# Kernel tuning notes

Measured on AMD Instinct MI355X. Metric: run time of the kernel, lower is better.

Reference implementation:

```python
import jax, jax.numpy as jnp
import numpy as np

# Dimensions (see shape_source)
L = 1024   # episode_len (memory slots)
B = 64     # batch (parallel envs)
K = 512    # key_size
V = 512    # value_size
H = 8      # num_head
MEMB = 256 # memory_state_embedding
SDIM = 512 # state_dim
HID = 512  # hidden width of all 2-layer encoders
RIMQ = 512 # rim_query_size
LAT = K - MEMB  # task_inference_latent dim


def setup_inputs() -> dict:
    key = jax.random.key(0)
    ks = jax.random.split(key, 16)
    w = lambda k, shape: (jax.random.normal(k, shape, jnp.float32) * 0.02)
    return {
        "state": jax.random.normal(ks[0], (B, SDIM), jnp.float32),
        "task_inference_latent": jax.random.normal(ks[1], (B, LAT), jnp.float32),
        "keys": jax.random.normal(ks[2], (L, B, K), jnp.float32),
        "vals": jax.random.normal(ks[3], (L, B, V), jnp.float32),
        "rpe_mod": jax.random.uniform(ks[4], (L, B, 1), jnp.float32),
        "step": jnp.maximum(jax.random.randint(ks[5], (B,), 0, L), 1),
        "W_state": w(ks[6], (SDIM, MEMB)), "b_state": jnp.zeros((MEMB,), jnp.float32),
        "Wcq1": w(ks[7], (K, HID)), "bcq1": jnp.zeros((HID,), jnp.float32),
        "Wcq2": w(ks[8], (HID, K)), "bcq2": jnp.zeros((K,), jnp.float32),
        "Wq": w(ks[9], (K, H * K)), "bq": jnp.zeros((H * K,), jnp.float32),
        "Wagg": w(ks[10], (H * V, V)), "bagg": jnp.zeros((V,), jnp.float32),
        "Wrk1": w(ks[11], (V, HID)), "brk1": jnp.zeros((HID,), jnp.float32),
        "Wrk2": w(ks[12], (HID, RIMQ)), "brk2": jnp.zeros((RIMQ,), jnp.float32),
        "Wrv1": w(ks[13], (V, HID)), "brv1": jnp.zeros((HID,), jnp.float32),
        "Wrv2": w(ks[14], (HID, V)), "brv2": jnp.zeros((V,), jnp.float32),
    }


def reference(state, task_inference_latent, keys, vals, rpe_mod, step,
              W_state, b_state, Wcq1, bcq1, Wcq2, bcq2, Wq, bq, Wagg, bagg,
              Wrk1, brk1, Wrk2, brk2, Wrv1, brv1, Wrv2, brv2):
    # DND.read (exploration branch), vectorized over the batch loop.
    se = state @ W_state + b_state                         # state_encoder: [B, MEMB]
    q = jnp.concatenate([se, task_inference_latent], -1)   # [B, K]
    # concat_query_encoder: stacked Linears with NO nonlinearity (faithful to source)
    q = (q @ Wcq1 + bcq1) @ Wcq2 + bcq2                    # [B, K]
    q = (q @ Wq + bq).reshape(B, H, K)                     # multi-head queries

    mk = keys * rpe_mod                                    # RPE-modulated keys [L, B, K]
    scores = jnp.einsum('lbk,bhk->blh', mk, q) / jnp.sqrt(jnp.float32(K))  # [B, L, H]
    valid = jnp.arange(L)[None, :] < step[:, None]         # [B, L] only slots < step[i]
    scores = jnp.where(valid[:, :, None], scores, jnp.float32(-1e30))
    prob = jax.nn.softmax(scores, axis=1) * valid[:, :, None].astype(scores.dtype)

    result = jnp.einsum('blh,lbv->bhv', prob, vals).reshape(B, H * V)
    result = (result @ Wagg + bagg)[:, None, :]            # value_aggregator -> [B, 1, V]
    out_key = (result @ Wrk1 + brk1) @ Wrk2 + brk2         # read_memory_to_key  [B, 1, RIMQ]
    out_val = (result @ Wrv1 + brv1) @ Wrv2 + brv2         # read_memory_to_value [B, 1, V]
    return out_key, out_val
```

## Files before the change

### kernel.cpp

```cpp
#include <hip/hip_runtime.h>
#include <math.h>

#define F4(p)  (*reinterpret_cast<float4*>(p))
#define CF4(p) (*reinterpret_cast<const float4*>(p))

#define ROWS  32
#define MAXC  32

__device__ __forceinline__ void gemm_core(
    const float* __restrict__ Asrc, const float* __restrict__ inbias,
    const float* __restrict__ til,
    int NS, int srcld, int kc, int k0,
    const float* __restrict__ W, int ldw, int n0,
    const float* __restrict__ obias, float* __restrict__ Pout, int ldo)
{
    __shared__ float As[16*64], Ws[16*64];
    const int t = threadIdx.x;
    const int tx = t & 15, ty = t >> 4;
    const int row = t >> 2, kq = (t & 3) * 4;
    const int wrow = t >> 4, wcol = (t & 15) * 4;
    float acc[4][4] = {};
    for (int kk = 0; kk < kc; kk += 16) {
        const int kg = k0 + kk + kq;
        float4 av;
        if (til && kg >= 256) {
            av = CF4(&til[row*256 + (kg - 256)]);
        } else {
            av = {0.f, 0.f, 0.f, 0.f};
            if (inbias) av = CF4(&inbias[kg]);
            for (int s = 0; s < NS; ++s) {
                float4 v = CF4(&Asrc[(size_t)(s*64 + row)*srcld + kg]);
                av.x += v.x; av.y += v.y; av.z += v.z; av.w += v.w;
            }
        }
        As[(kq+0)*64+row] = av.x; As[(kq+1)*64+row] = av.y;
        As[(kq+2)*64+row] = av.z; As[(kq+3)*64+row] = av.w;
        F4(&Ws[wrow*64 + wcol]) = CF4(&W[(size_t)(k0 + kk + wrow)*ldw + n0 + wcol]);
        __syncthreads();
        #pragma unroll
        for (int k = 0; k < 16; ++k) {
            float4 a4 = CF4(&As[k*64 + ty*4]);
            float4 w4 = CF4(&Ws[k*64 + tx*4]);
            float a[4] = {a4.x, a4.y, a4.z, a4.w};
            float w[4] = {w4.x, w4.y, w4.z, w4.w};
            #pragma unroll
            for (int i = 0; i < 4; ++i)
                #pragma unroll
                for (int j = 0; j < 4; ++j)
                    acc[i][j] += a[i] * w[j];
        }
        __syncthreads();
    }
    #pragma unroll
    for (int i = 0; i < 4; ++i) {
        float4 o = {acc[i][0], acc[i][1], acc[i][2], acc[i][3]};
        if (obias) {
            float4 ob = CF4(&obias[n0 + tx*4]);
            o.x += ob.x; o.y += ob.y; o.z += ob.z; o.w += ob.w;
        }
        F4(&Pout[(size_t)(ty*4 + i)*ldo + n0 + tx*4]) = o;
    }
}

__global__ __launch_bounds__(256) void k_q1(
    const float* __restrict__ state, const float* __restrict__ W_state,
    float* __restrict__ P1)
{
    const int nt = blockIdx.x, ks = blockIdx.y;
    gemm_core(state, nullptr, nullptr, 1, 512, 64, ks*64,
              W_state, 256, nt*64, nullptr, P1 + (size_t)ks*64*256, 256);
}

__global__ __launch_bounds__(256) void k_q2(
    const float* __restrict__ P1, const float* __restrict__ b_state,
    const float* __restrict__ til, const float* __restrict__ Wcq1,
    float* __restrict__ P2)
{
    const int nt = blockIdx.x, ks = blockIdx.y;
    gemm_core(P1, b_state, til, 8, 256, 64, ks*64,
              Wcq1, 512, nt*64, nullptr, P2 + (size_t)ks*64*512, 512);
}

__global__ __launch_bounds__(256) void k_q3(
    const float* __restrict__ P2, const float* __restrict__ bcq1,
    const float* __restrict__ Wcq2, float* __restrict__ P3)
{
    const int nt = blockIdx.x, ks = blockIdx.y;
    gemm_core(P2, bcq1, nullptr, 8, 512, 64, ks*64,
              Wcq2, 512, nt*64, nullptr, P3 + (size_t)ks*64*512, 512);
}

__global__ __launch_bounds__(256) void k_qh(
    const float* __restrict__ P3, const float* __restrict__ bcq2,
    const float* __restrict__ Wq, float* __restrict__ P4)
{
    const int nt = blockIdx.x, ks = blockIdx.y;
    gemm_core(P3, bcq2, nullptr, 8, 512, 128, ks*128,
              Wq, 4096, nt*64, nullptr, P4 + (size_t)ks*64*4096, 4096);
}

__global__ __launch_bounds__(256) void k_qsum(
    const float* __restrict__ P4, const float* __restrict__ bq,
    float* __restrict__ qh)
{
    const int b = blockIdx.x, t = threadIdx.x;
    #pragma unroll
    for (int j = 0; j < 4; ++j) {
        int f = t + j*256;
        float4 v = CF4(&bq[f*4]);
        #pragma unroll
        for (int s = 0; s < 4; ++s) {
            float4 u = CF4(&P4[(size_t)(s*64 + b)*4096 + f*4]);
            v.x += u.x; v.y += u.y; v.z += u.z; v.w += u.w;
        }
        F4(&qh[(size_t)b*4096 + f*4]) = v;
    }
}

__global__ __launch_bounds__(256, 4) void k_fa(
    const float* __restrict__ keys, const float* __restrict__ rpe,
    const float* __restrict__ qh, const float* __restrict__ vals,
    const int* __restrict__ step,
    float* __restrict__ Facc, float* __restrict__ Fms)
{
    __shared__ float s_q[4096];
    __shared__ float s_sc[ROWS*8];
    __shared__ float red[256];
    __shared__ float s_m[8];
    const int b = blockIdx.y, lc = blockIdx.x;
    const int sb = step[b];
    const int l0 = lc * ROWS;
    if (l0 >= sb) return;
    const int nl = min(ROWS, sb - l0);
    const int t = threadIdx.x;
    float* facc_out = Facc + ((size_t)(lc*64) + b)*4096;

    for (int i = t; i < 1024; i += 256)
        F4(&s_q[i*4]) = CF4(&qh[(size_t)b*4096 + i*4]);
    __syncthreads();
    const int lane = t & 63, w = t >> 6;
    float qr[8][8];
    #pragma unroll
    for (int h = 0; h < 8; ++h) {
        float4 x = CF4(&s_q[h*512 + lane*8]);
        float4 y = CF4(&s_q[h*512 + lane*8 + 4]);
        qr[h][0]=x.x; qr[h][1]=x.y; qr[h][2]=x.z; qr[h][3]=x.w;
        qr[h][4]=y.x; qr[h][5]=y.y; qr[h][6]=y.z; qr[h][7]=y.w;
    }
    const float inv_sqrtK = 0.04419417382415922f;
    const bool p0 = lane & 1, p1 = lane & 2, p2 = lane & 4;
    const size_t kstride = (size_t)4*64*512;
    const float* kp = keys + ((size_t)(l0 + w)*64 + b)*512 + lane*8;
    float4 k0x, k0y, k1x, k1y;
    if (w < nl)     { k0x = CF4(kp);           k0y = CF4(kp + 4); }
    if (w + 4 < nl) { k1x = CF4(kp + kstride); k1y = CF4(kp + kstride + 4); }
    for (int il = w; il < nl; il += 4) {
        float kv[8] = {k0x.x,k0x.y,k0x.z,k0x.w, k0y.x,k0y.y,k0y.z,k0y.w};
        k0x = k1x; k0y = k1y;
        if (il + 8 < nl) { k1x = CF4(kp + 2*kstride); k1y = CF4(kp + 2*kstride + 4); }
        kp += kstride;
        float pr[8] = {};
        #pragma unroll
        for (int h = 0; h < 8; ++h)
            #pragma unroll
            for (int j = 0; j < 8; ++j)
                pr[h] += kv[j] * qr[h][j];
        float w4[4], x2[2], y;
        #pragma unroll
        for (int i = 0; i < 4; ++i) {
            float keep = p0 ? pr[2*i+1] : pr[2*i];
            float send = p0 ? pr[2*i]   : pr[2*i+1];
            w4[i] = keep + __shfl_xor(send, 1);
        }
        #pragma unroll
        for (int i = 0; i < 2; ++i) {
            float keep = p1 ? w4[2*i+1] : w4[2*i];
            float send = p1 ? w4[2*i]   : w4[2*i+1];
            x2[i] = keep + __shfl_xor(send, 2);
        }
        {
            float keep = p2 ? x2[1] : x2[0];
            float send = p2 ? x2[0] : x2[1];
            y = keep + __shfl_xor(send, 4);
        }
        y += __shfl_xor(y, 8);
        y += __shfl_xor(y, 16);
        y += __shfl_xor(y, 32);
        if (lane < 8)
            s_sc[il*8 + lane] = y * rpe[(l0 + il)*64 + b] * inv_sqrtK;
    }
    __syncthreads();
    const int h = t & 7, g = t >> 3;
    float m = -1e30f;
    for (int l = g; l < nl; l += 32) m = fmaxf(m, s_sc[l*8 + h]);
    red[g*8 + h] = m;
    __syncthreads();
    #pragma unroll
    for (int s = 16; s; s >>= 1) {
        if (g < s) red[g*8+h] = fmaxf(red[g*8+h], red[(g+s)*8+h]);
        __syncthreads();
    }
    if (t < 8) s_m[t] = red[t];
    __syncthreads();
    float mh = s_m[h], s_acc = 0.f;
    for (int l = g; l < nl; l += 32) {
        float e = __expf(s_sc[l*8 + h] - mh);
        s_sc[l*8 + h] = e;
        s_acc += e;
    }
    red[g*8 + h] = s_acc;
    __syncthreads();
    #pragma unroll
    for (int s = 16; s; s >>= 1) {
        if (g < s) red[g*8+h] += red[(g+s)*8+h];
        __syncthreads();
    }
    if (t < 8) {
        size_t o = ((size_t)(lc*64 + b)*8 + t)*2;
        Fms[o] = s_m[t]; Fms[o+1] = red[t];
    }
    const int par = t >> 7, c = t & 127;
    float4 acc[8] = {};
    const size_t vstride = (size_t)2*64*512;
    const float* vp = vals + ((size_t)(l0 + par)*64 + b)*512 + c*4;
    float4 v0, v1, v2;
    if (par < nl)     v0 = CF4(vp);
    if (par + 2 < nl) v1 = CF4(vp + vstride);
    if (par + 4 < nl) v2 = CF4(vp + 2*vstride);
    for (int il = par; il < nl; il += 2) {
        float4 pa = CF4(&s_sc[il*8]);
        float4 pb = CF4(&s_sc[il*8 + 4]);
        acc[0].x += pa.x*v0.x; acc[0].y += pa.x*v0.y; acc[0].z += pa.x*v0.z; acc[0].w += pa.x*v0.w;
        acc[1].x += pa.y*v0.x; acc[1].y += pa.y*v0.y; acc[1].z += pa.y*v0.z; acc[1].w += pa.y*v0.w;
        acc[2].x += pa.z*v0.x; acc[2].y += pa.z*v0.y; acc[2].z += pa.z*v0.z; acc[2].w += pa.z*v0.w;
        acc[3].x += pa.w*v0.x; acc[3].y += pa.w*v0.y; acc[3].z += pa.w*v0.z; acc[3].w += pa.w*v0.w;
        acc[4].x += pb.x*v0.x; acc[4].y += pb.x*v0.y; acc[4].z += pb.x*v0.z; acc[4].w += pb.x*v0.w;
        acc[5].x += pb.y*v0.x; acc[5].y += pb.y*v0.y; acc[5].z += pb.y*v0.z; acc[5].w += pb.y*v0.w;
        acc[6].x += pb.z*v0.x; acc[6].y += pb.z*v0.y; acc[6].z += pb.z*v0.z; acc[6].w += pb.z*v0.w;
        acc[7].x += pb.w*v0.x; acc[7].y += pb.w*v0.y; acc[7].z += pb.w*v0.z; acc[7].w += pb.w*v0.w;
        v0 = v1; v1 = v2;
        if (il + 6 < nl) v2 = CF4(vp + 3*vstride);
        vp += vstride;
    }
    __syncthreads();
    if (par == 1) {
        #pragma unroll
        for (int hh = 0; hh < 8; ++hh)
            F4(&s_q[(c*8 + hh)*4]) = acc[hh];
    }
    __syncthreads();
    if (par == 0) {
        #pragma unroll
        for (int hh = 0; hh < 8; ++hh) {
            float4 o = CF4(&s_q[(c*8 + hh)*4]);
            o.x += acc[hh].x; o.y += acc[hh].y; o.z += acc[hh].z; o.w += acc[hh].w;
            F4(&facc_out[hh*512 + c*4]) = o;
        }
    }
}

__global__ __launch_bounds__(256) void k_comb(
    const float* __restrict__ Facc, const float* __restrict__ Fms,
    const int* __restrict__ step, float* __restrict__ res)
{
    __shared__ float wgt[MAXC*8];
    __shared__ float s_inv[8];
    const int b = blockIdx.x, t = threadIdx.x;
    const int nc = (step[b] + ROWS - 1) / ROWS;
    if (t < 8) {
        float M = -1e30f;
        for (int i = 0; i < nc; ++i)
            M = fmaxf(M, Fms[((size_t)(i*64 + b)*8 + t)*2]);
        float D = 0.f;
        for (int i = 0; i < nc; ++i) {
            size_t o = ((size_t)(i*64 + b)*8 + t)*2;
            float e = __expf(Fms[o] - M);
            wgt[i*8 + t] = e;
            D += e * Fms[o+1];
        }
        s_inv[t] = 1.f / D;
    }
    __syncthreads();
    #pragma unroll
    for (int j = 0; j < 4; ++j) {
        int f = t + j*256;
        int h = f >> 7;
        float4 a = {0.f, 0.f, 0.f, 0.f};
        for (int i = 0; i < nc; ++i) {
            float wi = wgt[i*8 + h];
            float4 v = CF4(&Facc[((size_t)(i*64) + b)*4096 + f*4]);
            a.x += wi*v.x; a.y += wi*v.y; a.z += wi*v.z; a.w += wi*v.w;
        }
        float inv = s_inv[h];
        a.x *= inv; a.y *= inv; a.z *= inv; a.w *= inv;
        F4(&res[(size_t)b*4096 + f*4]) = a;
    }
}

__global__ __launch_bounds__(256) void k_agg(
    const float* __restrict__ res, const float* __restrict__ Wagg,
    float* __restrict__ P5)
{
    const int nt = blockIdx.x, ks = blockIdx.y;
    gemm_core(res, nullptr, nullptr, 1, 4096, 128, ks*128,
              Wagg, 512, nt*64, nullptr, P5 + (size_t)ks*64*512, 512);
}

__global__ __launch_bounds__(256) void k_rkv1(
    const float* __restrict__ P5, const float* __restrict__ bagg,
    const float* __restrict__ Wrk1, const float* __restrict__ Wrv1,
    float* __restrict__ P6)
{
    const int nt = blockIdx.x, ks = blockIdx.y, z = blockIdx.z;
    gemm_core(P5, bagg, nullptr, 32, 512, 128, ks*128,
              z ? Wrv1 : Wrk1, 512, nt*64,
              nullptr, P6 + (size_t)(z*4 + ks)*64*512, 512);
}

__global__ __launch_bounds__(256) void k_rkv2(
    const float* __restrict__ P6,
    const float* __restrict__ brk1, const float* __restrict__ brv1,
    const float* __restrict__ Wrk2, const float* __restrict__ Wrv2,
    const float* __restrict__ brk2, const float* __restrict__ brv2,
    float* __restrict__ out)
{
    const int nt = blockIdx.x, z = blockIdx.z;
    gemm_core(P6 + (size_t)z*4*64*512, z ? brv1 : brk1, nullptr, 4, 512, 512, 0,
              z ? Wrv2 : Wrk2, 512, nt*64,
              z ? brv2 : brk2, out + (size_t)z*64*512, 512);
}

extern "C" void kernel_launch(void* const* d_in, const int* in_sizes, int n_in,
                              void* d_out, int out_size, void* d_ws, size_t ws_size,
                              hipStream_t stream) {
    const float* state   = (const float*)d_in[0];
    const float* til     = (const float*)d_in[1];
    const float* keys    = (const float*)d_in[2];
    const float* vals    = (const float*)d_in[3];
    const float* rpe     = (const float*)d_in[4];
    const int*   step    = (const int*)d_in[5];
    const float* W_state = (const float*)d_in[6];
    const float* b_state = (const float*)d_in[7];
    const float* Wcq1 = (const float*)d_in[8];
    const float* bcq1 = (const float*)d_in[9];
    const float* Wcq2 = (const float*)d_in[10];
    const float* bcq2 = (const float*)d_in[11];
    const float* Wq   = (const float*)d_in[12];
    const float* bq   = (const float*)d_in[13];
    const float* Wagg = (const float*)d_in[14];
    const float* bagg = (const float*)d_in[15];
    const float* Wrk1 = (const float*)d_in[16];
    const float* brk1 = (const float*)d_in[17];
    const float* Wrk2 = (const float*)d_in[18];
    const float* brk2 = (const float*)d_in[19];
    const float* Wrv1 = (const float*)d_in[20];
    const float* brv1 = (const float*)d_in[21];
    const float* Wrv2 = (const float*)d_in[22];
    const float* brv2 = (const float*)d_in[23];
    float* out = (float*)d_out;
    float* ws  = (float*)d_ws;

    float* P1   = ws;
    float* P2   = ws + 131072;
    float* P3   = ws + 393216;
    float* P4   = ws + 655360;
    float* qh   = ws + 1703936;
    float* Facc = ws + 1966080;
    float* Fms  = ws + 10354688;
    float* res  = ws + 10387456;
    float* P5   = ws;
    float* P6   = ws + 1048576;

    k_q1  <<<dim3(4,8),   256, 0, stream>>>(state, W_state, P1);
    k_q2  <<<dim3(8,8),   256, 0, stream>>>(P1, b_state, til, Wcq1, P2);
    k_q3  <<<dim3(8,8),   256, 0, stream>>>(P2, bcq1, Wcq2, P3);
    k_qh  <<<dim3(64,4),  256, 0, stream>>>(P3, bcq2, Wq, P4);
    k_qsum<<<64, 256, 0, stream>>>(P4, bq, qh);
    k_fa  <<<dim3(MAXC,64), 256, 0, stream>>>(keys, rpe, qh, vals, step, Facc, Fms);
    k_comb<<<64, 256, 0, stream>>>(Facc, Fms, step, res);
    k_agg <<<dim3(8,32),  256, 0, stream>>>(res, Wagg, P5);
    k_rkv1<<<dim3(8,4,2), 256, 0, stream>>>(P5, bagg, Wrk1, Wrv1, P6);
    k_rkv2<<<dim3(8,1,2), 256, 0, stream>>>(P6, brk1, brv1, Wrk2, Wrv2,
                                            brk2, brv2, out);
}
```

Before: 181.8 us.

## Map one wave per batch in flash-read and split rows evenly by step

The attention-read kernel now gives each wavefront one batch element, four per block. Each batch quad's valid range is split into 32 even chunks sized by the quad's maximum step, instead of fixed 32-row chunks that leave many blocks idle. Block-wide shared-memory reductions and __syncthreads are replaced by wave shuffles. Keys and values are prefetched four rows deep, and the combine kernel skips empty chunks. In exchange the grid is a quarter the size, so fewer waves are resident to hide memory latency, and rows are re-read at chunk tails because addresses are clamped.

```diff
diff --git a/kernel.cpp b/kernel.cpp
--- a/kernel.cpp
+++ b/kernel.cpp
@@ -4,8 +4,7 @@
 #define F4(p)  (*reinterpret_cast<float4*>(p))
 #define CF4(p) (*reinterpret_cast<const float4*>(p))
 
-#define ROWS  32
-#define MAXC  32
+#define NC 32
 
 __device__ __forceinline__ void gemm_core(
     const float* __restrict__ Asrc, const float* __restrict__ inbias,
@@ -117,48 +116,52 @@
     }
 }
 
-__global__ __launch_bounds__(256, 4) void k_fa(
+__global__ __launch_bounds__(256, 2) void k_fa(
     const float* __restrict__ keys, const float* __restrict__ rpe,
     const float* __restrict__ qh, const float* __restrict__ vals,
     const int* __restrict__ step,
     float* __restrict__ Facc, float* __restrict__ Fms)
 {
-    __shared__ float s_q[4096];
-    __shared__ float s_sc[ROWS*8];
-    __shared__ float red[256];
-    __shared__ float s_m[8];
-    const int b = blockIdx.y, lc = blockIdx.x;
+    __shared__ __align__(16) float s_sc[4][36*8];
+    __shared__ float s_rpe[4][32];
+    const int lc = blockIdx.x, bq = blockIdx.y;
+    const int t = threadIdx.x;
+    const int w = t >> 6, lane = t & 63;
+    const int b = bq*4 + w;
+    const int b0q = bq*4;
+    const int sbq = max(max(step[b0q], step[b0q+1]), max(step[b0q+2], step[b0q+3]));
+    const int l0 = (lc * sbq) >> 5;
+    const int l1 = ((lc + 1) * sbq) >> 5;
     const int sb = step[b];
-    const int l0 = lc * ROWS;
-    if (l0 >= sb) return;
-    const int nl = min(ROWS, sb - l0);
-    const int t = threadIdx.x;
-    float* facc_out = Facc + ((size_t)(lc*64) + b)*4096;
-
-    for (int i = t; i < 1024; i += 256)
-        F4(&s_q[i*4]) = CF4(&qh[(size_t)b*4096 + i*4]);
-    __syncthreads();
-    const int lane = t & 63, w = t >> 6;
+    const int nl = min(l1, sb) - l0;
+    if (nl <= 0) return;
+
+    const float inv_sqrtK = 0.04419417382415922f;
+    if (lane < nl) s_rpe[w][lane] = rpe[(l0 + lane)*64 + b] * inv_sqrtK;
+
     float qr[8][8];
-    #pragma unroll
-    for (int h = 0; h < 8; ++h) {
-        float4 x = CF4(&s_q[h*512 + lane*8]);
-        float4 y = CF4(&s_q[h*512 + lane*8 + 4]);
-        qr[h][0]=x.x; qr[h][1]=x.y; qr[h][2]=x.z; qr[h][3]=x.w;
-        qr[h][4]=y.x; qr[h][5]=y.y; qr[h][6]=y.z; qr[h][7]=y.w;
-    }
-    const float inv_sqrtK = 0.04419417382415922f;
+    {
+        const float* qb = qh + (size_t)b*4096 + lane*8;
+        #pragma unroll
+        for (int h = 0; h < 8; ++h) {
+            float4 x = CF4(&qb[h*512]);
+            float4 y = CF4(&qb[h*512 + 4]);
+            qr[h][0]=x.x; qr[h][1]=x.y; qr[h][2]=x.z; qr[h][3]=x.w;
+            qr[h][4]=y.x; qr[h][5]=y.y; qr[h][6]=y.z; qr[h][7]=y.w;
+        }
+    }
     const bool p0 = lane & 1, p1 = lane & 2, p2 = lane & 4;
-    const size_t kstride = (size_t)4*64*512;
-    const float* kp = keys + ((size_t)(l0 + w)*64 + b)*512 + lane*8;
-    float4 k0x, k0y, k1x, k1y;
-    if (w < nl)     { k0x = CF4(kp);           k0y = CF4(kp + 4); }
-    if (w + 4 < nl) { k1x = CF4(kp + kstride); k1y = CF4(kp + kstride + 4); }
-    for (int il = w; il < nl; il += 4) {
-        float kv[8] = {k0x.x,k0x.y,k0x.z,k0x.w, k0y.x,k0y.y,k0y.z,k0y.w};
-        k0x = k1x; k0y = k1y;
-        if (il + 8 < nl) { k1x = CF4(kp + 2*kstride); k1y = CF4(kp + 2*kstride + 4); }
-        kp += kstride;
+    const size_t RS = (size_t)64*512;
+
+    const float* kbase = keys + ((size_t)l0*64 + b)*512 + lane*8;
+    auto kaddr = [&](int r) { return kbase + (size_t)min(r, nl-1)*RS; };
+    float4 k0x = CF4(kaddr(0)), k0y = CF4(kaddr(0)+4);
+    float4 k1x = CF4(kaddr(1)), k1y = CF4(kaddr(1)+4);
+    float4 k2x = CF4(kaddr(2)), k2y = CF4(kaddr(2)+4);
+    float4 k3x = CF4(kaddr(3)), k3y = CF4(kaddr(3)+4);
+    auto score_step = [&](float4& bx, float4& by, int r) {
+        float kv[8] = {bx.x,bx.y,bx.z,bx.w, by.x,by.y,by.z,by.w};
+        bx = CF4(kaddr(r+4)); by = CF4(kaddr(r+4)+4);
         float pr[8] = {};
         #pragma unroll
         for (int h = 0; h < 8; ++h)
@@ -167,16 +170,16 @@
                 pr[h] += kv[j] * qr[h][j];
         float w4[4], x2[2], y;
         #pragma unroll
-        for (int i = 0; i < 4; ++i) {
-            float keep = p0 ? pr[2*i+1] : pr[2*i];
-            float send = p0 ? pr[2*i]   : pr[2*i+1];
-            w4[i] = keep + __shfl_xor(send, 1);
-        }
-        #pragma unroll
-        for (int i = 0; i < 2; ++i) {
-            float keep = p1 ? w4[2*i+1] : w4[2*i];
-            float send = p1 ? w4[2*i]   : w4[2*i+1];
-            x2[i] = keep + __shfl_xor(send, 2);
+        for (int q = 0; q < 4; ++q) {
+            float keep = p0 ? pr[2*q+1] : pr[2*q];
+            float send = p0 ? pr[2*q]   : pr[2*q+1];
+            w4[q] = keep + __shfl_xor(send, 1);
+        }
+        #pragma unroll
+        for (int q = 0; q < 2; ++q) {
+            float keep = p1 ? w4[2*q+1] : w4[2*q];
+            float send = p1 ? w4[2*q]   : w4[2*q+1];
+            x2[q] = keep + __shfl_xor(send, 2);
         }
         {
             float keep = p2 ? x2[1] : x2[0];
@@ -186,76 +189,68 @@
         y += __shfl_xor(y, 8);
         y += __shfl_xor(y, 16);
         y += __shfl_xor(y, 32);
-        if (lane < 8)
-            s_sc[il*8 + lane] = y * rpe[(l0 + il)*64 + b] * inv_sqrtK;
-    }
-    __syncthreads();
-    const int h = t & 7, g = t >> 3;
+        if (r < nl && lane < 8) s_sc[w][r*8 + lane] = y * s_rpe[w][r];
+    };
+    for (int r = 0; r < nl; r += 4) {
+        score_step(k0x, k0y, r);
+        score_step(k1x, k1y, r + 1);
+        score_step(k2x, k2y, r + 2);
+        score_step(k3x, k3y, r + 3);
+    }
+
+    const int h = lane & 7, rg = lane >> 3;
     float m = -1e30f;
-    for (int l = g; l < nl; l += 32) m = fmaxf(m, s_sc[l*8 + h]);
-    red[g*8 + h] = m;
-    __syncthreads();
+    for (int r = rg; r < nl; r += 8) m = fmaxf(m, s_sc[w][r*8 + h]);
+    m = fmaxf(m, __shfl_xor(m, 8));
+    m = fmaxf(m, __shfl_xor(m, 16));
+    m = fmaxf(m, __shfl_xor(m, 32));
+    float sacc = 0.f;
+    for (int r = rg; r < nl; r += 8) {
+        float e = __expf(s_sc[w][r*8 + h] - m);
+        s_sc[w][r*8 + h] = e;
+        sacc += e;
+    }
+    if (rg < 4) s_sc[w][(nl + rg)*8 + h] = 0.f;
+    sacc += __shfl_xor(sacc, 8);
+    sacc += __shfl_xor(sacc, 16);
+    sacc += __shfl_xor(sacc, 32);
+    if (lane < 8) {
+        size_t o = ((size_t)(lc*64 + b)*8 + lane)*2;
+        Fms[o] = m; Fms[o+1] = sacc;
+    }
+
+    float4 accA[8] = {}, accB[8] = {};
+    const float* vbase = vals + ((size_t)l0*64 + b)*512 + lane*8;
+    auto vaddr = [&](int r) { return vbase + (size_t)min(r, nl-1)*RS; };
+    float4 v0a = CF4(vaddr(0)), v0b = CF4(vaddr(0)+4);
+    float4 v1a = CF4(vaddr(1)), v1b = CF4(vaddr(1)+4);
+    float4 v2a = CF4(vaddr(2)), v2b = CF4(vaddr(2)+4);
+    float4 v3a = CF4(vaddr(3)), v3b = CF4(vaddr(3)+4);
+    auto pv_step = [&](float4& va, float4& vb, int r) {
+        float4 a4 = va, b4 = vb;
+        va = CF4(vaddr(r+4)); vb = CF4(vaddr(r+4)+4);
+        float4 pa = CF4(&s_sc[w][r*8]);
+        float4 pb = CF4(&s_sc[w][r*8 + 4]);
+        float p[8] = {pa.x, pa.y, pa.z, pa.w, pb.x, pb.y, pb.z, pb.w};
+        #pragma unroll
+        for (int hh = 0; hh < 8; ++hh) {
+            accA[hh].x += p[hh]*a4.x; accA[hh].y += p[hh]*a4.y;
+            accA[hh].z += p[hh]*a4.z; accA[hh].w += p[hh]*a4.w;
+            accB[hh].x += p[hh]*b4.x; accB[hh].y += p[hh]*b4.y;
+            accB[hh].z += p[hh]*b4.z; accB[hh].w += p[hh]*b4.w;
+        }
+    };
+    for (int r = 0; r < nl; r += 4) {
+        pv_step(v0a, v0b, r);
+        pv_step(v1a, v1b, r + 1);
+        pv_step(v2a, v2b, r + 2);
+        pv_step(v3a, v3b, r + 3);
+    }
+    float* fout = Facc + ((size_t)(lc*64) + b)*4096 + lane*8;
     #pragma unroll
-    for (int s = 16; s; s >>= 1) {
-        if (g < s) red[g*8+h] = fmaxf(red[g*8+h], red[(g+s)*8+h]);
-        __syncthreads();
-    }
-    if (t < 8) s_m[t] = red[t];
-    __syncthreads();
-    float mh = s_m[h], s_acc = 0.f;
-    for (int l = g; l < nl; l += 32) {
-        float e = __expf(s_sc[l*8 + h] - mh);
-        s_sc[l*8 + h] = e;
-        s_acc += e;
-    }
-    red[g*8 + h] = s_acc;
-    __syncthreads();
-    #pragma unroll
-    for (int s = 16; s; s >>= 1) {
-        if (g < s) red[g*8+h] += red[(g+s)*8+h];
-        __syncthreads();
-    }
-    if (t < 8) {
-        size_t o = ((size_t)(lc*64 + b)*8 + t)*2;
-        Fms[o] = s_m[t]; Fms[o+1] = red[t];
-    }
-    const int par = t >> 7, c = t & 127;
-    float4 acc[8] = {};
-    const size_t vstride = (size_t)2*64*512;
-    const float* vp = vals + ((size_t)(l0 + par)*64 + b)*512 + c*4;
-    float4 v0, v1, v2;
-    if (par < nl)     v0 = CF4(vp);
-    if (par + 2 < nl) v1 = CF4(vp + vstride);
-    if (par + 4 < nl) v2 = CF4(vp + 2*vstride);
-    for (int il = par; il < nl; il += 2) {
-        float4 pa = CF4(&s_sc[il*8]);
-        float4 pb = CF4(&s_sc[il*8 + 4]);
-        acc[0].x += pa.x*v0.x; acc[0].y += pa.x*v0.y; acc[0].z += pa.x*v0.z; acc[0].w += pa.x*v0.w;
-        acc[1].x += pa.y*v0.x; acc[1].y += pa.y*v0.y; acc[1].z += pa.y*v0.z; acc[1].w += pa.y*v0.w;
-        acc[2].x += pa.z*v0.x; acc[2].y += pa.z*v0.y; acc[2].z += pa.z*v0.z; acc[2].w += pa.z*v0.w;
-        acc[3].x += pa.w*v0.x; acc[3].y += pa.w*v0.y; acc[3].z += pa.w*v0.z; acc[3].w += pa.w*v0.w;
-        acc[4].x += pb.x*v0.x; acc[4].y += pb.x*v0.y; acc[4].z += pb.x*v0.z; acc[4].w += pb.x*v0.w;
-        acc[5].x += pb.y*v0.x; acc[5].y += pb.y*v0.y; acc[5].z += pb.y*v0.z; acc[5].w += pb.y*v0.w;
-        acc[6].x += pb.z*v0.x; acc[6].y += pb.z*v0.y; acc[6].z += pb.z*v0.z; acc[6].w += pb.z*v0.w;
-        acc[7].x += pb.w*v0.x; acc[7].y += pb.w*v0.y; acc[7].z += pb.w*v0.z; acc[7].w += pb.w*v0.w;
-        v0 = v1; v1 = v2;
-        if (il + 6 < nl) v2 = CF4(vp + 3*vstride);
-        vp += vstride;
-    }
-    __syncthreads();
-    if (par == 1) {
-        #pragma unroll
-        for (int hh = 0; hh < 8; ++hh)
-            F4(&s_q[(c*8 + hh)*4]) = acc[hh];
-    }
-    __syncthreads();
-    if (par == 0) {
-        #pragma unroll
-        for (int hh = 0; hh < 8; ++hh) {
-            float4 o = CF4(&s_q[(c*8 + hh)*4]);
-            o.x += acc[hh].x; o.y += acc[hh].y; o.z += acc[hh].z; o.w += acc[hh].w;
-            F4(&facc_out[hh*512 + c*4]) = o;
-        }
+    for (int hh = 0; hh < 8; ++hh) {
+        F4(&fout[hh*512])     = accA[hh];
+        F4(&fout[hh*512 + 4]) = accB[hh];
     }
 }
 
@@ -263,20 +258,29 @@
     const float* __restrict__ Facc, const float* __restrict__ Fms,
     const int* __restrict__ step, float* __restrict__ res)
 {
-    __shared__ float wgt[MAXC*8];
+    __shared__ float wgt[NC*8];
     __shared__ float s_inv[8];
     const int b = blockIdx.x, t = threadIdx.x;
-    const int nc = (step[b] + ROWS - 1) / ROWS;
+    const int b0q = b & ~3;
+    const int sbq = max(max(step[b0q], step[b0q+1]), max(step[b0q+2], step[b0q+3]));
+    const int sb = step[b];
     if (t < 8) {
         float M = -1e30f;
-        for (int i = 0; i < nc; ++i)
-            M = fmaxf(M, Fms[((size_t)(i*64 + b)*8 + t)*2]);
+        for (int i = 0; i < NC; ++i) {
+            int L0 = (i*sbq) >> 5, L1 = ((i+1)*sbq) >> 5;
+            if (min(L1, sb) - L0 > 0)
+                M = fmaxf(M, Fms[((size_t)(i*64 + b)*8 + t)*2]);
+        }
         float D = 0.f;
-        for (int i = 0; i < nc; ++i) {
-            size_t o = ((size_t)(i*64 + b)*8 + t)*2;
-            float e = __expf(Fms[o] - M);
+        for (int i = 0; i < NC; ++i) {
+            int L0 = (i*sbq) >> 5, L1 = ((i+1)*sbq) >> 5;
+            float e = 0.f;
+            if (min(L1, sb) - L0 > 0) {
+                size_t o = ((size_t)(i*64 + b)*8 + t)*2;
+                e = __expf(Fms[o] - M);
+                D += e * Fms[o+1];
+            }
             wgt[i*8 + t] = e;
-            D += e * Fms[o+1];
         }
         s_inv[t] = 1.f / D;
     }
@@ -286,10 +290,12 @@
         int f = t + j*256;
         int h = f >> 7;
         float4 a = {0.f, 0.f, 0.f, 0.f};
-        for (int i = 0; i < nc; ++i) {
+        for (int i = 0; i < NC; ++i) {
             float wi = wgt[i*8 + h];
-            float4 v = CF4(&Facc[((size_t)(i*64) + b)*4096 + f*4]);
-            a.x += wi*v.x; a.y += wi*v.y; a.z += wi*v.z; a.w += wi*v.w;
+            if (wi != 0.f) {
+                float4 v = CF4(&Facc[((size_t)(i*64) + b)*4096 + f*4]);
+                a.x += wi*v.x; a.y += wi*v.y; a.z += wi*v.z; a.w += wi*v.w;
+            }
         }
         float inv = s_inv[h];
         a.x *= inv; a.y *= inv; a.z *= inv; a.w *= inv;
@@ -376,7 +382,7 @@
     k_q3  <<<dim3(8,8),   256, 0, stream>>>(P2, bcq1, Wcq2, P3);
     k_qh  <<<dim3(64,4),  256, 0, stream>>>(P3, bcq2, Wq, P4);
     k_qsum<<<64, 256, 0, stream>>>(P4, bq, qh);
-    k_fa  <<<dim3(MAXC,64), 256, 0, stream>>>(keys, rpe, qh, vals, step, Facc, Fms);
+    k_fa  <<<dim3(NC,16), 256, 0, stream>>>(keys, rpe, qh, vals, step, Facc, Fms);
     k_comb<<<64, 256, 0, stream>>>(Facc, Fms, step, res);
     k_agg <<<dim3(8,32),  256, 0, stream>>>(res, Wagg, P5);
     k_rkv1<<<dim3(8,4,2), 256, 0, stream>>>(P5, bagg, Wrk1, Wrv1, P6);
```

New measurement: 202.1 us. +11.1%, slower.
